# Kernel tuning notes

Hardware: AMD Instinct MI355X
Metric: run time of the kernel (lower is better)

The kernel has to match this reference:

```python
import jax, jax.numpy as jnp
import numpy as np

T_SZ, T_STEP, T_CUT = 9, 6, 2
B, N, C, FS = 4, 2048, 512, 1
GRID = 120


def setup_inputs() -> dict:
    key = jax.random.key(0)
    rng = np.random.default_rng(0)
    ys = np.empty((B, N), np.int64)
    xs = np.empty((B, N), np.int64)
    for b in range(B):
        cells = rng.permutation(GRID * GRID)[:N]  # unique cells -> deterministic scatter
        ys[b] = cells // GRID
        xs[b] = cells % GRID
    features = jax.random.uniform(key, (B, N, C, FS, FS), jnp.float32)
    return {"features": features, "ys": jnp.asarray(ys), "xs": jnp.asarray(xs)}


def reference(features, ys, xs):
    # Faithful eager translation of TiledFeaturesMap.forward with validation=True
    # (y_rnd = x_rnd = 0, no random flips/transposes).
    f_tiles_list, f_ns_list = [], []
    for b in range(features.shape[0]):
        r = ys[b] > -1
        yv = ys[b][r]
        xv = xs[b][r]
        fv = features[b][r]                         # [nv, C, FS, FS]
        y_min, y_max = int(yv.min()), int(yv.max())
        x_min, x_max = int(xv.min()), int(xv.max())
        H = y_max - y_min + 1 + T_SZ
        W = x_max - x_min + 1 + T_SZ
        x_map = jnp.zeros((H, W, C, FS, FS), features.dtype).at[yv - y_min, xv - x_min].set(fv)
        nH = (H - T_SZ) // T_STEP + 1
        nW = (W - T_SZ) // T_STEP + 1
        ih = (jnp.arange(nH) * T_STEP)[:, None] + jnp.arange(T_SZ)[None, :]  # [nH, T_SZ]
        iw = (jnp.arange(nW) * T_STEP)[:, None] + jnp.arange(T_SZ)[None, :]  # [nW, T_SZ]
        # gather windows: [nH, nW, T_SZ, T_SZ, C, FS, FS]
        tiles = x_map[ih[:, None, :, None], iw[None, :, None, :]]
        # match torch unfold layout [nH, nW, C, FS, FS, T_SZ, T_SZ]
        tiles = tiles.transpose(0, 1, 4, 5, 6, 2, 3)
        center = tiles[..., T_CUT:-T_CUT, T_CUT:-T_CUT]
        sums = center.reshape(nH, nW, -1).sum(-1)
        mask = sums > 0
        if not bool(mask.any()):
            sums = tiles.reshape(nH, nW, -1).sum(-1)
            mask = sums > 0
        sel = tiles[mask]                            # [nt, C, FS, FS, T_SZ, T_SZ]
        f_tiles_list.append(sel)
        f_ns_list += [b] * int(mask.sum())
    f_tiles = jnp.concatenate(f_tiles_list, axis=0)
    f_ns = jnp.asarray(np.array(f_ns_list, np.int64))
    # permute(0,1,4,2,5,3): [Nt,C,FS,FS,T,T] -> [Nt,C,T,FS,T,FS] -> [Nt,C,T*FS,T*FS]
    f_tiles = f_tiles.transpose(0, 1, 4, 2, 5, 3).reshape(f_tiles.shape[0], C, T_SZ * FS, T_SZ * FS)
    return (f_ns, f_tiles)
```

## Files before the change

### kernel.cpp

```cpp
#include <hip/hip_runtime.h>
#include <hip/hip_bf16.h>
#include <limits.h>

#define BB   4
#define NN   2048
#define CC   512
#define TSZ  9
#define TSTEP 6
#define TCUT 2
#define GRIDW 120
#define CMS  132
#define CMSZ (CMS * CMS)
#define TILE_ELEMS (CC * TSZ * TSZ)
#define OUT_PER_TILE (TILE_ELEMS + 1)
#define TI_STRIDE 448

__device__ __forceinline__ void light_barrier() {
    asm volatile("s_waitcnt lgkmcnt(0)" ::: "memory");
    __builtin_amdgcn_s_barrier();
}

__global__ __launch_bounds__(512) void setup_kernel(
        const int* __restrict__ ys, const int* __restrict__ xs,
        int* __restrict__ cellmap, int* __restrict__ tinfo,
        int* __restrict__ counts) {
    const int b = blockIdx.x;
    const int tid = threadIdx.x;
    const int lane = tid & 63;
    const int wid = tid >> 6;
    __shared__ int s_red[8][4];
    __shared__ int s_bbox[4];
    __shared__ int s_wave[8];

    int* __restrict__ cm = cellmap + b * CMSZ;

    int4* __restrict__ cm4 = (int4*)cm;
    for (int i = tid; i < CMSZ / 4; i += 512) cm4[i] = make_int4(-1, -1, -1, -1);
    __syncthreads();

    int ymin = INT_MAX, ymax = INT_MIN, xmin = INT_MAX, xmax = INT_MIN;
    for (int j = tid; j < NN; j += 512) {
        int y = ys[b * NN + j], x = xs[b * NN + j];
        if (y > -1) {
            cm[y * CMS + x] = j;
            ymin = min(ymin, y); ymax = max(ymax, y);
            xmin = min(xmin, x); xmax = max(xmax, x);
        }
    }
    #pragma unroll
    for (int off = 32; off; off >>= 1) {
        ymin = min(ymin, __shfl_xor(ymin, off));
        ymax = max(ymax, __shfl_xor(ymax, off));
        xmin = min(xmin, __shfl_xor(xmin, off));
        xmax = max(xmax, __shfl_xor(xmax, off));
    }
    if (lane == 0) {
        s_red[wid][0] = ymin; s_red[wid][1] = ymax;
        s_red[wid][2] = xmin; s_red[wid][3] = xmax;
    }
    __syncthreads();
    if (tid == 0) {
        int a = INT_MAX, e = INT_MIN, c = INT_MAX, d = INT_MIN;
        for (int w = 0; w < 8; ++w) {
            a = min(a, s_red[w][0]); e = max(e, s_red[w][1]);
            c = min(c, s_red[w][2]); d = max(d, s_red[w][3]);
        }
        s_bbox[0] = a; s_bbox[1] = e; s_bbox[2] = c; s_bbox[3] = d;
    }
    __syncthreads();
    ymin = s_bbox[0]; ymax = s_bbox[1]; xmin = s_bbox[2]; xmax = s_bbox[3];

    int nH = (ymax - ymin + 1) / TSTEP + 1;
    int nW = (xmax - xmin + 1) / TSTEP + 1;
    int nT = nH * nW;

    bool m = false;
    int gy0 = 0, gx0 = 0;
    if (tid < nT) {
        int ti = tid / nW, tj = tid - ti * nW;
        gy0 = ymin + ti * TSTEP;
        gx0 = xmin + tj * TSTEP;
        const int* __restrict__ bp = cm + (gy0 + TCUT) * CMS + (gx0 + TCUT);
        int acc = -1;
        #pragma unroll
        for (int dy = 0; dy < 5; ++dy)
            #pragma unroll
            for (int dx = 0; dx < 5; ++dx)
                acc = max(acc, bp[dy * CMS + dx]);
        m = (acc >= 0);
    }
    unsigned long long bal = __ballot(m);
    int lpre = __popcll(bal & ((1ull << lane) - 1ull));
    if (lane == 0) s_wave[wid] = (int)__popcll(bal);
    __syncthreads();
    if (tid == 0) {
        int acc = 0;
        for (int w = 0; w < 8; ++w) { int v = s_wave[w]; s_wave[w] = acc; acc += v; }
        counts[b] = acc;
    }
    __syncthreads();
    if (m) tinfo[b * TI_STRIDE + s_wave[wid] + lpre] = (gy0 << 8) | gx0;
}

__global__ __launch_bounds__(256) void fill_kernel(
        const float* __restrict__ feats, const int* __restrict__ cellmap,
        const int* __restrict__ tinfo, const int* __restrict__ counts,
        float* __restrict__ f_ns, float* __restrict__ out_tiles) {
    __shared__ int s_list[81];
    __shared__ int s_wcnt[2];
    __shared__ int s_cnt;
    __shared__ __align__(16) float s_f[64 * 81];

    const int tid = threadIdx.x;
    const int lane = tid & 63;
    const int wid = tid >> 6;
    const int k = blockIdx.x >> 1;
    const int h = blockIdx.x & 1;

    int c0 = counts[0], c1 = counts[1], c2 = counts[2];
    int b, base;
    if (k < c0)                { b = 0; base = 0; }
    else if (k < c0 + c1)      { b = 1; base = c0; }
    else if (k < c0 + c1 + c2) { b = 2; base = c0 + c1; }
    else                       { b = 3; base = c0 + c1 + c2; }
    const int info = tinfo[b * TI_STRIDE + (k - base)];
    const int gy0 = info >> 8, gx0 = info & 255;
    if (tid == 0 && h == 0) f_ns[k] = (float)b;

    const float4 z = make_float4(0.f, 0.f, 0.f, 0.f);
    for (int f4 = tid; f4 < 1296; f4 += 256) ((float4*)s_f)[f4] = z;

    int n = -1;
    if (tid < 81) {
        int r = tid / 9, c = tid - r * 9;
        n = cellmap[b * CMSZ + (gy0 + r) * CMS + (gx0 + c)];
    }
    bool occ = (tid < 81) && (n >= 0);
    unsigned long long bal = __ballot(occ);
    int pre = __popcll(bal & ((1ull << lane) - 1ull));
    if (lane == 0 && wid < 2) s_wcnt[wid] = (int)__popcll(bal);
    __syncthreads();
    if (occ) s_list[(wid == 1 ? s_wcnt[0] : 0) + pre] = (n << 7) | tid;
    if (tid == 0) s_cnt = s_wcnt[0] + s_wcnt[1];
    __syncthreads();

    const int nk = s_cnt;
    const int items = nk * 16;
    const float* __restrict__ fb = feats + (size_t)b * (NN * CC) + h * 256;
    float* __restrict__ outk = out_tiles + (size_t)k * TILE_ELEMS + h * (4 * 64 * 81);

    if (items <= 512) {
        const bool h0 = tid < items, h1 = tid + 256 < items;
        const float* p0 = fb; const float* p1 = fb;
        int d0 = 0, d1 = 0;
        if (h0) { int pk = s_list[tid >> 4], q = tid & 15;
                  p0 = fb + (pk >> 7) * CC + q * 4; d0 = q * 324 + (pk & 127); }
        if (h1) { int e = tid + 256; int pk = s_list[e >> 4], q = e & 15;
                  p1 = fb + (pk >> 7) * CC + q * 4; d1 = q * 324 + (pk & 127); }
        float4 g0, g1;
        if (h0) g0 = *(const float4*)p0;
        if (h1) g1 = *(const float4*)p1;
        #pragma unroll 1
        for (int c = 0; c < 4; ++c) {
            if (h0) { s_f[d0] = g0.x; s_f[d0+81] = g0.y; s_f[d0+162] = g0.z; s_f[d0+243] = g0.w; }
            if (h1) { s_f[d1] = g1.x; s_f[d1+81] = g1.y; s_f[d1+162] = g1.z; s_f[d1+243] = g1.w; }
            light_barrier();
            if (c < 3) {
                if (h0) { p0 += 64; g0 = *(const float4*)p0; }
                if (h1) { p1 += 64; g1 = *(const float4*)p1; }
            }
            float* __restrict__ outc = outk + c * (64 * 81);
            #pragma unroll
            for (int it = 0; it < 6; ++it) {
                int idx = it * 256 + tid;
                if (idx < 1296) {
                    float4 v = ((const float4*)s_f)[idx];
                    *((float4*)outc + idx) = v;
                }
            }
            light_barrier();
        }
    } else {
        for (int c = 0; c < 4; ++c) {
            for (int e = tid; e < items; e += 256) {
                int pk = s_list[e >> 4], q = e & 15;
                float4 v = *(const float4*)(fb + (pk >> 7) * CC + c * 64 + q * 4);
                int d = q * 324 + (pk & 127);
                s_f[d] = v.x; s_f[d+81] = v.y; s_f[d+162] = v.z; s_f[d+243] = v.w;
            }
            light_barrier();
            float* __restrict__ outc = outk + c * (64 * 81);
            for (int f4 = tid; f4 < 1296; f4 += 256) {
                float4 v = ((const float4*)s_f)[f4];
                *((float4*)outc + f4) = v;
            }
            light_barrier();
        }
    }
}

extern "C" void kernel_launch(void* const* d_in, const int* in_sizes, int n_in,
                              void* d_out, int out_size, void* d_ws, size_t ws_size,
                              hipStream_t stream) {
    const float* feats = (const float*)d_in[0];
    const int* ys = (const int*)d_in[1];
    const int* xs = (const int*)d_in[2];
    float* out = (float*)d_out;

    char* ws = (char*)d_ws;
    int* cellmap = (int*)ws;
    int* tinfo = (int*)(ws + BB * CMSZ * 4);
    int* counts = (int*)(ws + BB * CMSZ * 4 + BB * TI_STRIDE * 4);

    const int K = out_size / OUT_PER_TILE;
    float* f_ns = out;
    float* out_tiles = out + K;

    setup_kernel<<<BB, 512, 0, stream>>>(ys, xs, cellmap, tinfo, counts);
    fill_kernel<<<K * 2, 256, 0, stream>>>(feats, cellmap, tinfo, counts, f_ns, out_tiles);
}
```

Before: 59.36 us.

## Align tile output stores and double-buffer LDS chunks in fill kernel

The tile region of the output starts at out+K, which is generally not 16-byte aligned, so the old float4 stores could be misaligned. The fill kernel now offsets the shared staging buffer by K mod 4 and writes a few scalar head and tail elements around aligned vector stores. The channel chunks are halved to 32 and staged through two alternating LDS buffers, which removes the second barrier per chunk. The cost is more loop iterations, with only one gather load per thread each, and extra scalar edge stores.

After: 62.61 us. 1.05x slower.

```diff
diff --git a/kernel.cpp b/kernel.cpp
--- a/kernel.cpp
+++ b/kernel.cpp
@@ -14,6 +14,9 @@
 #define TILE_ELEMS (CC * TSZ * TSZ)
 #define OUT_PER_TILE (TILE_ELEMS + 1)
 #define TI_STRIDE 448
+#define CHUNK_F 2592
+
+typedef float f32x4 __attribute__((ext_vector_type(4)));
 
 __device__ __forceinline__ void light_barrier() {
     asm volatile("s_waitcnt lgkmcnt(0)" ::: "memory");
@@ -105,11 +108,11 @@
 __global__ __launch_bounds__(256) void fill_kernel(
         const float* __restrict__ feats, const int* __restrict__ cellmap,
         const int* __restrict__ tinfo, const int* __restrict__ counts,
-        float* __restrict__ f_ns, float* __restrict__ out_tiles) {
+        float* __restrict__ out, int K) {
     __shared__ int s_list[81];
     __shared__ int s_wcnt[2];
     __shared__ int s_cnt;
-    __shared__ __align__(16) float s_f[64 * 81];
+    __shared__ __align__(16) float s_raw[2][CHUNK_F + 4];
 
     const int tid = threadIdx.x;
     const int lane = tid & 63;
@@ -125,10 +128,13 @@
     else                       { b = 3; base = c0 + c1 + c2; }
     const int info = tinfo[b * TI_STRIDE + (k - base)];
     const int gy0 = info >> 8, gx0 = info & 255;
-    if (tid == 0 && h == 0) f_ns[k] = (float)b;
-
-    const float4 z = make_float4(0.f, 0.f, 0.f, 0.f);
-    for (int f4 = tid; f4 < 1296; f4 += 256) ((float4*)s_f)[f4] = z;
+    if (tid == 0 && h == 0) out[k] = (float)b;
+
+    {
+        f32x4* z4 = (f32x4*)&s_raw[0][0];
+        const f32x4 z = {0.f, 0.f, 0.f, 0.f};
+        for (int i = tid; i < 2 * (CHUNK_F + 4) / 4; i += 256) z4[i] = z;
+    }
 
     int n = -1;
     if (tid < 81) {
@@ -145,56 +151,66 @@
     __syncthreads();
 
     const int nk = s_cnt;
-    const int items = nk * 16;
+    const int items = nk * 8;
     const float* __restrict__ fb = feats + (size_t)b * (NN * CC) + h * 256;
-    float* __restrict__ outk = out_tiles + (size_t)k * TILE_ELEMS + h * (4 * 64 * 81);
-
-    if (items <= 512) {
-        const bool h0 = tid < items, h1 = tid + 256 < items;
-        const float* p0 = fb; const float* p1 = fb;
-        int d0 = 0, d1 = 0;
-        if (h0) { int pk = s_list[tid >> 4], q = tid & 15;
-                  p0 = fb + (pk >> 7) * CC + q * 4; d0 = q * 324 + (pk & 127); }
-        if (h1) { int e = tid + 256; int pk = s_list[e >> 4], q = e & 15;
-                  p1 = fb + (pk >> 7) * CC + q * 4; d1 = q * 324 + (pk & 127); }
-        float4 g0, g1;
-        if (h0) g0 = *(const float4*)p0;
-        if (h1) g1 = *(const float4*)p1;
+
+    const int off = K & 3;
+    const int mh  = (4 - off) & 3;
+    const int nf4 = (mh == 0) ? (CHUNK_F / 4) : (CHUNK_F / 4 - 1);
+    const int mt  = off;
+    const size_t Fbase = (size_t)K + (size_t)k * TILE_ELEMS + (size_t)h * (8 * CHUNK_F);
+
+    if (nk <= 32) {
+        const bool hv = tid < items;
+        const float* p = fb;
+        int d = 0;
+        if (hv) {
+            int pk = s_list[tid >> 3], q = tid & 7;
+            p = fb + (pk >> 7) * CC + q * 4;
+            d = off + q * 4 * 81 + (pk & 127);
+        }
+        f32x4 g;
+        if (hv) g = *(const f32x4*)p;
         #pragma unroll 1
-        for (int c = 0; c < 4; ++c) {
-            if (h0) { s_f[d0] = g0.x; s_f[d0+81] = g0.y; s_f[d0+162] = g0.z; s_f[d0+243] = g0.w; }
-            if (h1) { s_f[d1] = g1.x; s_f[d1+81] = g1.y; s_f[d1+162] = g1.z; s_f[d1+243] = g1.w; }
+        for (int cc = 0; cc < 8; ++cc) {
+            float* __restrict__ sb = s_raw[cc & 1];
+            if (hv) { sb[d] = g.x; sb[d+81] = g.y; sb[d+162] = g.z; sb[d+243] = g.w; }
             light_barrier();
-            if (c < 3) {
-                if (h0) { p0 += 64; g0 = *(const float4*)p0; }
-                if (h1) { p1 += 64; g1 = *(const float4*)p1; }
+            if (cc < 7 && hv) { p += 32; g = *(const f32x4*)p; }
+            float* __restrict__ outc = out + Fbase + cc * CHUNK_F;
+            const float* __restrict__ sr = sb + off;
+            if (tid < mh) outc[tid] = sr[tid];
+            const f32x4* __restrict__ s4 = (const f32x4*)(sb + off + mh);
+            f32x4* __restrict__ o4 = (f32x4*)(outc + mh);
+            #pragma unroll
+            for (int it = 0; it < 3; ++it) {
+                int idx = it * 256 + tid;
+                if (idx < nf4) o4[idx] = s4[idx];
             }
-            float* __restrict__ outc = outk + c * (64 * 81);
-            #pragma unroll
-            for (int it = 0; it < 6; ++it) {
-                int idx = it * 256 + tid;
-                if (idx < 1296) {
-                    float4 v = ((const float4*)s_f)[idx];
-                    *((float4*)outc + idx) = v;
-                }
+            if (tid < mt) outc[mh + 4 * nf4 + tid] = sr[mh + 4 * nf4 + tid];
+        }
+    } else {
+        #pragma unroll 1
+        for (int cc = 0; cc < 8; ++cc) {
+            float* __restrict__ sb = s_raw[cc & 1];
+            for (int e = tid; e < items; e += 256) {
+                int pk = s_list[e >> 3], q = e & 7;
+                f32x4 g = *(const f32x4*)(fb + (pk >> 7) * CC + cc * 32 + q * 4);
+                int d = off + q * 4 * 81 + (pk & 127);
+                sb[d] = g.x; sb[d+81] = g.y; sb[d+162] = g.z; sb[d+243] = g.w;
             }
             light_barrier();
-        }
-    } else {
-        for (int c = 0; c < 4; ++c) {
-            for (int e = tid; e < items; e += 256) {
-                int pk = s_list[e >> 4], q = e & 15;
-                float4 v = *(const float4*)(fb + (pk >> 7) * CC + c * 64 + q * 4);
-                int d = q * 324 + (pk & 127);
-                s_f[d] = v.x; s_f[d+81] = v.y; s_f[d+162] = v.z; s_f[d+243] = v.w;
+            float* __restrict__ outc = out + Fbase + cc * CHUNK_F;
+            const float* __restrict__ sr = sb + off;
+            if (tid < mh) outc[tid] = sr[tid];
+            const f32x4* __restrict__ s4 = (const f32x4*)(sb + off + mh);
+            f32x4* __restrict__ o4 = (f32x4*)(outc + mh);
+            #pragma unroll
+            for (int it = 0; it < 3; ++it) {
+                int idx = it * 256 + tid;
+                if (idx < nf4) o4[idx] = s4[idx];
             }
-            light_barrier();
-            float* __restrict__ outc = outk + c * (64 * 81);
-            for (int f4 = tid; f4 < 1296; f4 += 256) {
-                float4 v = ((const float4*)s_f)[f4];
-                *((float4*)outc + f4) = v;
-            }
-            light_barrier();
+            if (tid < mt) outc[mh + 4 * nf4 + tid] = sr[mh + 4 * nf4 + tid];
         }
     }
 }
@@ -213,9 +229,7 @@
     int* counts = (int*)(ws + BB * CMSZ * 4 + BB * TI_STRIDE * 4);
 
     const int K = out_size / OUT_PER_TILE;
-    float* f_ns = out;
-    float* out_tiles = out + K;
 
     setup_kernel<<<BB, 512, 0, stream>>>(ys, xs, cellmap, tinfo, counts);
-    fill_kernel<<<K * 2, 256, 0, stream>>>(feats, cellmap, tinfo, counts, f_ns, out_tiles);
-}
+    fill_kernel<<<K * 2, 256, 0, stream>>>(feats, cellmap, tinfo, counts, out, K);
+}
```
